# Kernel tuning notes

Hardware: AMD Instinct MI355X
Metric: run time of the kernel (lower is better)

The kernel has to match this reference:

```python
import jax, jax.numpy as jnp
import numpy as np

B, N, M, D = 2, 16384, 4096, 128  # batch, points, voxels, d_model (= d_points)


def _mlp(x, W1, b1, W2, b2):
    # Linear -> ReLU -> Linear (matches nn.Sequential(Linear, ReLU, Linear))
    return jax.nn.relu(x @ W1 + b1) @ W2 + b2


def setup_inputs() -> dict:
    key = jax.random.key(0)
    ks = jax.random.split(key, 12)
    s = 0.02
    inp = {
        "p_xyz": jax.random.normal(ks[0], (B, N, 3), jnp.float32),
        "v_xyz": jax.random.normal(ks[1], (B, 3), jnp.float32),
        "p_features": jax.random.normal(ks[2], (B, N, D), jnp.float32),
        "v_featrues": jax.random.normal(ks[3], (B, M, D), jnp.float32),
    }

    def two_layer(k, din):
        k1, k2 = jax.random.split(k)
        return (jax.random.normal(k1, (din, D), jnp.float32) * s,
                jnp.zeros((D,), jnp.float32),
                jax.random.normal(k2, (D, D), jnp.float32) * s,
                jnp.zeros((D,), jnp.float32))

    for name, din, k in (("alpha", D, ks[4]), ("beta", D, ks[5]),
                         ("omega", D, ks[6]), ("delta", 3, ks[7])):
        W1, b1, W2, b2 = two_layer(k, din)
        inp[name + "_W1"] = W1
        inp[name + "_b1"] = b1
        inp[name + "_W2"] = W2
        inp[name + "_b2"] = b2
    return inp


def reference(p_xyz, v_xyz, p_features, v_featrues,
              alpha_W1, alpha_b1, alpha_W2, alpha_b2,
              beta_W1, beta_b1, beta_W2, beta_b2,
              omega_W1, omega_b1, omega_W2, omega_b2,
              delta_W1, delta_b1, delta_W2, delta_b2):
    # dist = |p_xyz - v_xyz| per batch: [B, N, 3]
    dist = jnp.abs(p_xyz - v_xyz[:, None, :])
    pv = _mlp(dist, delta_W1, delta_b1, delta_W2, delta_b2)        # [B, N, D]
    q = _mlp(v_featrues, alpha_W1, alpha_b1, alpha_W2, alpha_b2)   # [B, M, D]
    k = _mlp(p_features, beta_W1, beta_b1, beta_W2, beta_b2)       # [B, N, D]
    v = _mlp(p_features, omega_W1, omega_b1, omega_W2, omega_b2)   # [B, N, D]
    # q@k^T + q@pv^T == q@(k+pv)^T : [B, M, N]
    scale = 1.0 / jnp.sqrt(jnp.asarray(D, dtype=q.dtype))
    scores = jnp.einsum('bmd,bnd->bmn', q, k + pv) * scale
    # softmax over dim=-2 (the query/voxel dim M), as in the original
    w = jax.nn.softmax(scores, axis=-2)                            # [B, M, N]
    res = jnp.einsum('bmn,bnd->bmd', w, v)                         # [B, M, D]
    return res + v_featrues
```

## Files before the change

### kernel.cpp

```cpp
#include <hip/hip_runtime.h>

#define B_ 2
#define N_ 16384
#define M_ 4096
#define D_ 128

typedef __attribute__((ext_vector_type(8))) short s8;
typedef __attribute__((ext_vector_type(4))) float f4;
typedef __attribute__((ext_vector_type(16))) float f16v;
typedef __attribute__((ext_vector_type(4))) unsigned short us4;
typedef unsigned short u16;

__device__ __forceinline__ u16 f2b(float f) {
  unsigned int x = __float_as_uint(f);
  unsigned int r = x + 0x7fffu + ((x >> 16) & 1u);
  return (u16)(r >> 16);
}
__device__ __forceinline__ s8 ld8(const u16* p) {
  return *reinterpret_cast<const s8*>(p);
}
__device__ __forceinline__ s8 ldcvt8(const float* p) {
  f4 x = *reinterpret_cast<const f4*>(p);
  f4 y = *reinterpret_cast<const f4*>(p + 4);
  s8 r;
  r[0] = (short)f2b(x[0]); r[1] = (short)f2b(x[1]);
  r[2] = (short)f2b(x[2]); r[3] = (short)f2b(x[3]);
  r[4] = (short)f2b(y[0]); r[5] = (short)f2b(y[1]);
  r[6] = (short)f2b(y[2]); r[7] = (short)f2b(y[3]);
  return r;
}
__device__ __forceinline__ f4 mfma16(s8 a, s8 b, f4 c) {
  return __builtin_amdgcn_mfma_f32_16x16x32_bf16(a, b, c, 0, 0, 0);
}
__device__ __forceinline__ f16v mfma32(s8 a, s8 b, f16v c) {
  return __builtin_amdgcn_mfma_f32_32x32x16_bf16(a, b, c, 0, 0, 0);
}
__device__ __forceinline__ int swz(int row, int off) {
  return (row << 8) + ((((off >> 4) ^ (row & 15)) << 4) | (off & 15));
}
#define CS 0.1275174365f

__device__ __forceinline__ void lds_barrier() {
  asm volatile("s_waitcnt lgkmcnt(0)" ::: "memory");
  __builtin_amdgcn_s_barrier();
}

__global__ __launch_bounds__(256) void wtrans(
    const float* a0, const float* a1, const float* a2, const float* a3,
    const float* a4, const float* a5, const float* a6, u16* dst) {
  const int mat = blockIdx.x >> 4, part = blockIdx.x & 15;
  const float* s;
  switch (mat) {
    case 0: s = a0; break; case 1: s = a1; break; case 2: s = a2; break;
    case 3: s = a3; break; case 4: s = a4; break; case 5: s = a5; break;
    default: s = a6; break;
  }
  u16* d = dst + mat * 16384 + part * 1024;
  const int o0 = part * 1024;
  for (int i = threadIdx.x; i < 1024; i += 256) {
    const int o = o0 + i;
    const int c = o >> 7, r = o & 127;
    d[i] = f2b(s[r * 128 + c]);
  }
}

__global__ __launch_bounds__(256) void mlps(
    const float* __restrict__ vfeat,
    const u16* __restrict__ aW1t, const float* __restrict__ ab1,
    const u16* __restrict__ aW2t, const float* __restrict__ ab2,
    u16* __restrict__ qbuf,
    const float* __restrict__ pf, const float* __restrict__ pxyz,
    const float* __restrict__ vxyz,
    const u16* __restrict__ bW1t, const float* __restrict__ bb1,
    const u16* __restrict__ bW2t, const float* __restrict__ bb2,
    const float* __restrict__ dW1, const float* __restrict__ db1,
    const u16* __restrict__ dW2t, const float* __restrict__ db2,
    const u16* __restrict__ oW1t, const float* __restrict__ ob1,
    const u16* __restrict__ oW2t, const float* __restrict__ ob2,
    u16* __restrict__ kpv_out, u16* __restrict__ vt_out) {
  __shared__ u16 H1[64][136];
  __shared__ u16 H2[64][136];
  __shared__ u16 H3[64][136];
  const int tid = threadIdx.x;
  const int wave = tid >> 6, lane = tid & 63;
  const int c16 = lane & 15, quad = lane >> 4;

  if (blockIdx.x < 256) {
    const int rowg = wave & 1, nsh = wave >> 1;
    const long row0 = (long)blockIdx.x * 32 + rowg * 16;
    s8 a[4];
    {
      const float* xr = vfeat + (row0 + c16) * D_ + quad * 8;
      #pragma unroll
      for (int kk = 0; kk < 4; kk++) a[kk] = ldcvt8(xr + kk * 32);
    }
    #pragma unroll
    for (int ns = 0; ns < 4; ns++) {
      f4 acc = {0.f, 0.f, 0.f, 0.f};
      const int c = (nsh * 4 + ns) * 16 + c16;
      const u16* wr = aW1t + (long)c * 128 + quad * 8;
      #pragma unroll
      for (int kk = 0; kk < 4; kk++) acc = mfma16(a[kk], ld8(wr + kk * 32), acc);
      const float bias = ab1[c];
      #pragma unroll
      for (int r = 0; r < 4; r++) {
        float v = acc[r] + bias;
        H1[rowg * 16 + quad * 4 + r][c] = f2b(v > 0.f ? v : 0.f);
      }
    }
    __syncthreads();
    s8 a2[4];
    #pragma unroll
    for (int kk = 0; kk < 4; kk++)
      a2[kk] = *reinterpret_cast<const s8*>(&H1[rowg * 16 + c16][kk * 32 + quad * 8]);
    #pragma unroll
    for (int ns = 0; ns < 4; ns++) {
      f4 acc = {0.f, 0.f, 0.f, 0.f};
      const int c = (nsh * 4 + ns) * 16 + c16;
      const u16* wr = aW2t + (long)c * 128 + quad * 8;
      #pragma unroll
      for (int kk = 0; kk < 4; kk++) acc = mfma16(a2[kk], ld8(wr + kk * 32), acc);
      const float bias = ab2[c];
      #pragma unroll
      for (int r = 0; r < 4; r++)
        qbuf[(row0 + quad * 4 + r) * D_ + c] = f2b(acc[r] + bias);
    }
    return;
  }
  const int bx = blockIdx.x - 256;
  const long row0 = (long)bx * 64 + wave * 16;
  s8 a[4];
  {
    const float* xr = pf + (row0 + c16) * D_ + quad * 8;
    #pragma unroll
    for (int kk = 0; kk < 4; kk++) a[kk] = ldcvt8(xr + kk * 32);
  }
  #pragma unroll
  for (int ns = 0; ns < 8; ns++) {
    f4 accb = {0.f, 0.f, 0.f, 0.f}, acco = {0.f, 0.f, 0.f, 0.f};
    const int c = ns * 16 + c16;
    const u16* wrb = bW1t + (long)c * 128 + quad * 8;
    const u16* wro = oW1t + (long)c * 128 + quad * 8;
    #pragma unroll
    for (int kk = 0; kk < 4; kk++) {
      accb = mfma16(a[kk], ld8(wrb + kk * 32), accb);
      acco = mfma16(a[kk], ld8(wro + kk * 32), acco);
    }
    const float biasb = bb1[c], biaso = ob1[c];
    #pragma unroll
    for (int r = 0; r < 4; r++) {
      float vb = accb[r] + biasb;
      float vo = acco[r] + biaso;
      H1[wave * 16 + quad * 4 + r][c] = f2b(vb > 0.f ? vb : 0.f);
      H3[wave * 16 + quad * 4 + r][c] = f2b(vo > 0.f ? vo : 0.f);
    }
  }
  {
    const long bat = ((long)bx * 64) / N_;
    const float vx0 = vxyz[bat * 3 + 0];
    const float vx1 = vxyz[bat * 3 + 1];
    const float vx2 = vxyz[bat * 3 + 2];
    for (int i = 0; i < 32; i++) {
      const int e = lane + 64 * i;
      const int rr = e >> 7, cc = e & 127;
      const long gr = row0 + rr;
      const float d0 = fabsf(pxyz[gr * 3 + 0] - vx0);
      const float d1 = fabsf(pxyz[gr * 3 + 1] - vx1);
      const float d2 = fabsf(pxyz[gr * 3 + 2] - vx2);
      float h = d0 * dW1[cc] + d1 * dW1[128 + cc] + d2 * dW1[256 + cc] + db1[cc];
      H2[wave * 16 + rr][cc] = f2b(h > 0.f ? h : 0.f);
    }
  }
  __syncthreads();
  s8 ab[4], ad[4], ao[4];
  #pragma unroll
  for (int kk = 0; kk < 4; kk++) {
    ab[kk] = *reinterpret_cast<const s8*>(&H1[wave * 16 + c16][kk * 32 + quad * 8]);
    ad[kk] = *reinterpret_cast<const s8*>(&H2[wave * 16 + c16][kk * 32 + quad * 8]);
    ao[kk] = *reinterpret_cast<const s8*>(&H3[wave * 16 + c16][kk * 32 + quad * 8]);
  }
  #pragma unroll
  for (int ns = 0; ns < 8; ns++) {
    const int c = ns * 16 + c16;
    f4 acck = {0.f, 0.f, 0.f, 0.f};
    f4 accv = {0.f, 0.f, 0.f, 0.f};
    const u16* wrb = bW2t + (long)c * 128 + quad * 8;
    const u16* wrd = dW2t + (long)c * 128 + quad * 8;
    const u16* wro = oW2t + (long)c * 128 + quad * 8;
    #pragma unroll
    for (int kk = 0; kk < 4; kk++) {
      acck = mfma16(ab[kk], ld8(wrb + kk * 32), acck);
      acck = mfma16(ad[kk], ld8(wrd + kk * 32), acck);
      accv = mfma16(ao[kk], ld8(wro + kk * 32), accv);
    }
    const float biask = bb2[c] + db2[c];
    const float biasv = ob2[c];
    #pragma unroll
    for (int r = 0; r < 4; r++)
      kpv_out[(row0 + quad * 4 + r) * D_ + c] = f2b(acck[r] + biask);
    {
      const long g = row0 + quad * 4;
      const long bb = g >> 14;
      const long n = g & (N_ - 1);
      us4 pk;
      #pragma unroll
      for (int r = 0; r < 4; r++) pk[r] = f2b(accv[r] + biasv);
      *reinterpret_cast<us4*>(vt_out + bb * (long)128 * N_ + (long)c * N_ + n) = pk;
    }
  }
}

__global__ __launch_bounds__(512, 6) void colsum_v2c(const u16* __restrict__ q,
    const u16* __restrict__ kpv, float* __restrict__ sums) {
  __shared__ char LQ[16384];
  const int tid = threadIdx.x;
  const int wave = tid >> 6, lane = tid & 63;
  const int c16 = lane & 15, quad = lane >> 4;
  const int mh = blockIdx.x & 3;
  const int nb = ((blockIdx.x >> 2) & 127) * 128 + wave * 16;
  const int b = blockIdx.x >> 9;
  const int rsub = lane >> 4, ch = lane & 15;

  s8 ak[4];
  {
    const u16* kr = kpv + ((long)b * N_ + nb + c16) * D_ + quad * 8;
    #pragma unroll
    for (int kk = 0; kk < 4; kk++) ak[kk] = ld8(kr + kk * 32);
  }
  f4 sum = {0.f, 0.f, 0.f, 0.f};
  const u16* qb = q + (long)b * M_ * D_ + (long)mh * (M_ / 4) * D_;

  for (int m0 = 0; m0 < M_ / 4; m0 += 64) {
    s8 t0 = ld8(qb + (long)(m0 + wave * 8 + rsub) * D_ + ch * 8);
    s8 t1 = ld8(qb + (long)(m0 + wave * 8 + 4 + rsub) * D_ + ch * 8);
    *reinterpret_cast<s8*>(LQ + swz(wave * 8 + rsub, ch * 16)) = t0;
    *reinterpret_cast<s8*>(LQ + swz(wave * 8 + 4 + rsub, ch * 16)) = t1;
    __syncthreads();
    #pragma unroll
    for (int ms = 0; ms < 4; ms++) {
      f4 st = {0.f, 0.f, 0.f, 0.f};
      #pragma unroll
      for (int kk = 0; kk < 4; kk++) {
        s8 bq = *reinterpret_cast<const s8*>(LQ + swz(ms * 16 + c16, kk * 64 + quad * 16));
        st = mfma16(ak[kk], bq, st);
      }
      #pragma unroll
      for (int r = 0; r < 4; r++) sum[r] += exp2f(st[r] * CS);
    }
    __syncthreads();
  }
  #pragma unroll
  for (int mask = 1; mask < 16; mask <<= 1) {
    #pragma unroll
    for (int r = 0; r < 4; r++) sum[r] += __shfl_xor(sum[r], mask, 64);
  }
  if (c16 == 0)
    *reinterpret_cast<f4*>(sums + (long)mh * (B_ * N_) + (long)b * N_ + nb + quad * 4) = sum;
}

__global__ __launch_bounds__(256) void recip_k(const float* __restrict__ sums,
                                               float* __restrict__ l2ic) {
  const int i = blockIdx.x * 256 + threadIdx.x;
  const float s = sums[i] + sums[B_ * N_ + i] + sums[2 * B_ * N_ + i]
                + sums[3 * B_ * N_ + i];
  l2ic[i] = -log2f(s);
}

__global__ __launch_bounds__(256, 4) void attn_v10(const u16* __restrict__ q,
    const u16* __restrict__ kpv, const u16* __restrict__ vt,
    const float* __restrict__ l2ic, float* __restrict__ part,
    int lgns, int nslice) {
  __shared__ char LK[16384];
  __shared__ char LP[8192];
  const int tid = threadIdx.x;
  const int wave = tid >> 6, lane = tid & 63;
  const int l31 = lane & 31, hi = lane >> 5;
  const int bid = blockIdx.x;
  const int ns = bid & ((1 << lgns) - 1);
  const int mb = (bid >> lgns) & 63;
  const int b = bid >> (lgns + 6);
  const int nt = wave & 1, mt = wave >> 1;
  const int m_base = mb * 64;
  const int n_begin = ns * nslice;
  const int rsub = lane >> 4, ch = lane & 15;

  const u16* kpb = kpv + (long)b * N_ * D_;
  const u16* vtb = vt + (long)b * (long)D_ * N_;
  const float* l2b = l2ic + (long)b * N_;

  s8 bq[8];
  {
    const u16* qr = q + ((long)b * M_ + m_base + mt * 32 + l31) * D_ + hi * 8;
    #pragma unroll
    for (int kk = 0; kk < 8; kk++) bq[kk] = ld8(qr + kk * 16);
  }
  f16v acc[2];
  #pragma unroll
  for (int i = 0; i < 2; i++)
    #pragma unroll
    for (int r = 0; r < 16; r++) acc[i][r] = 0.f;

  s8 tmp[4];
  #pragma unroll
  for (int i = 0; i < 4; i++)
    tmp[i] = ld8(kpb + (long)(n_begin + wave * 16 + i * 4 + rsub) * D_ + ch * 8);

  for (int n0 = n_begin; n0 < n_begin + nslice; n0 += 64) {
    #pragma unroll
    for (int i = 0; i < 4; i++)
      *reinterpret_cast<s8*>(LK + swz(wave * 16 + i * 4 + rsub, ch * 16)) = tmp[i];
    {
      int nn = n0 + 64;
      if (nn >= n_begin + nslice) nn = n_begin;
      #pragma unroll
      for (int i = 0; i < 4; i++)
        tmp[i] = ld8(kpb + (long)(nn + wave * 16 + i * 4 + rsub) * D_ + ch * 8);
    }
    lds_barrier();
    {
      f16v st;
      #pragma unroll
      for (int r = 0; r < 16; r++) st[r] = 0.f;
      #pragma unroll
      for (int kk = 0; kk < 8; kk++) {
        s8 aK = *reinterpret_cast<const s8*>(
            LK + swz(nt * 32 + l31, kk * 32 + hi * 16));
        st = mfma32(aK, bq[kk], st);
      }
      #pragma unroll
      for (int g = 0; g < 4; g++) {
        const f4 l2 = *reinterpret_cast<const f4*>(l2b + n0 + nt * 32 + 8 * g + 4 * hi);
        us4 pk;
        #pragma unroll
        for (int r = 0; r < 4; r++)
          pk[r] = (u16)(__float_as_uint(exp2f(fmaf(st[g * 4 + r], CS, l2[r]))) >> 16);
        *reinterpret_cast<us4*>(LP + (4 * nt + g) * 1024 + (mt * 32 + l31) * 16 + 8 * hi) = pk;
      }
    }
    lds_barrier();
    #pragma unroll
    for (int kk = 0; kk < 4; kk++) {
      s8 bv = ld8(vtb + (long)(wave * 32 + l31) * N_ + n0 + kk * 16 + hi * 8);
      #pragma unroll
      for (int i = 0; i < 2; i++) {
        s8 ap = *reinterpret_cast<const s8*>(
            LP + (2 * kk + hi) * 1024 + (i * 32 + l31) * 16);
        acc[i] = mfma32(ap, bv, acc[i]);
      }
    }
  }
  float* pt = part + (long)bid * 64 * 128;
  #pragma unroll
  for (int i = 0; i < 2; i++)
    #pragma unroll
    for (int g = 0; g < 4; g++)
      #pragma unroll
      for (int r = 0; r < 4; r++)
        pt[(i * 32 + g * 8 + 4 * hi + r) * 128 + wave * 32 + l31] = acc[i][g * 4 + r];
}

__global__ __launch_bounds__(256) void attn_reduce(const float* __restrict__ part,
    const float* __restrict__ vfeat, float* __restrict__ out, int nsplit) {
  const int g4 = blockIdx.x * 256 + threadIdx.x;
  const int b = g4 >> 17;
  const int rem = g4 & 131071;
  const int m = rem >> 5;
  const int d4 = rem & 31;
  const int mb = m >> 6, mr = m & 63;
  const long base = ((long)(b * 64 + mb) * nsplit) * 8192 + mr * 128 + d4 * 4;
  f4 s = *reinterpret_cast<const f4*>(vfeat + (long)g4 * 4);
  for (int ns = 0; ns < nsplit; ns++)
    s += *reinterpret_cast<const f4*>(part + base + ns * 8192);
  *reinterpret_cast<f4*>(out + (long)g4 * 4) = s;
}

extern "C" void kernel_launch(void* const* d_in, const int* in_sizes, int n_in,
                              void* d_out, int out_size, void* d_ws, size_t ws_size,
                              hipStream_t stream) {
  const float* p_xyz  = (const float*)d_in[0];
  const float* v_xyz  = (const float*)d_in[1];
  const float* p_feat = (const float*)d_in[2];
  const float* v_feat = (const float*)d_in[3];
  const float* aW1 = (const float*)d_in[4],  *ab1 = (const float*)d_in[5];
  const float* aW2 = (const float*)d_in[6],  *ab2 = (const float*)d_in[7];
  const float* bW1 = (const float*)d_in[8],  *bb1 = (const float*)d_in[9];
  const float* bW2 = (const float*)d_in[10], *bb2 = (const float*)d_in[11];
  const float* oW1 = (const float*)d_in[12], *ob1 = (const float*)d_in[13];
  const float* oW2 = (const float*)d_in[14], *ob2 = (const float*)d_in[15];
  const float* dW1 = (const float*)d_in[16], *db1 = (const float*)d_in[17];
  const float* dW2 = (const float*)d_in[18], *db2 = (const float*)d_in[19];

  char* ws = (char*)d_ws;
  u16* wt    = (u16*)ws;
  u16* aW1t  = wt + 0 * 16384;
  u16* aW2t  = wt + 1 * 16384;
  u16* bW1t  = wt + 2 * 16384;
  u16* bW2t  = wt + 3 * 16384;
  u16* oW1t  = wt + 4 * 16384;
  u16* oW2t  = wt + 5 * 16384;
  u16* dW2t  = wt + 6 * 16384;
  u16* qbuf  = (u16*)(ws + 262144);
  u16* kpvb  = (u16*)(ws + 2359296);
  u16* vtb   = (u16*)(ws + 10747904);
  float* invb = (float*)(ws + 19136512);
  float* partb = (float*)(ws + 19267584);
  float* sums  = partb;

  const size_t part_off = 19267584;
  int lgns = (ws_size >= part_off + (size_t)8 * B_ * M_ * D_ * 4) ? 3 : 2;
  const int nsplit = 1 << lgns;
  const int nslice = N_ / nsplit;

  wtrans<<<dim3(112), dim3(256), 0, stream>>>(aW1, aW2, bW1, bW2, oW1, oW2, dW2, wt);
  mlps<<<dim3(256 + (B_ * N_) / 64), dim3(256), 0, stream>>>(
      v_feat, aW1t, ab1, aW2t, ab2, qbuf,
      p_feat, p_xyz, v_xyz, bW1t, bb1, bW2t, bb2, dW1, db1, dW2t, db2,
      oW1t, ob1, oW2t, ob2, kpvb, vtb);
  colsum_v2c<<<dim3(B_ * 128 * 4), dim3(512), 0, stream>>>(qbuf, kpvb, sums);
  recip_k<<<dim3((B_ * N_) / 256), dim3(256), 0, stream>>>(sums, invb);
  attn_v10<<<dim3(B_ * 64 * nsplit), dim3(256), 0, stream>>>(qbuf, kpvb, vtb, invb, partb,
                                                             lgns, nslice);
  attn_reduce<<<dim3((B_ * M_ * D_ / 4) / 256), dim3(256), 0, stream>>>(partb, v_feat,
                                                                        (float*)d_out,
                                                                        nsplit);
}
```

Baseline: 329.3 us.

## Double-buffer K tiles via direct global-to-LDS loads in attention kernel

Replaces the register-staged K tile copy with __builtin_amdgcn_global_load_lds into a double-buffered LDS array, prefetching two tiles ahead and synchronising with explicit vmcnt waits and barriers. It also hoists the l2ic loads before the QK MFMAs and batches the V loads before the PV MFMAs. The aim is to cut VGPR pressure and LDS write instructions and to overlap global latency with compute. LDS use per block doubles and the hand-counted vmcnt(4) wait is fragile: if it does not match the loads actually outstanding, reads can race.

```diff
diff --git a/kernel.cpp b/kernel.cpp
--- a/kernel.cpp
+++ b/kernel.cpp
@@ -266,11 +266,26 @@
   l2ic[i] = -log2f(s);
 }
 
-__global__ __launch_bounds__(256, 4) void attn_v10(const u16* __restrict__ q,
+#define STAGE_K(bufp, nn)                                                      \
+  {                                                                            \
+    _Pragma("unroll")                                                          \
+    for (int i_ = 0; i_ < 4; i_++) {                                           \
+      const int row_ = wave * 16 + i_ * 4 + rsub;                              \
+      const u16* src_ = kpb + (long)((nn) + row_) * D_ + ((ch ^ (row_ & 15)) * 8); \
+      char* dst_ = (bufp) + wave * 4096 + i_ * 1024;                           \
+      __builtin_amdgcn_global_load_lds(                                        \
+          (const __attribute__((address_space(1))) void*)src_,                 \
+          (__attribute__((address_space(3))) void*)dst_, 16, 0, 0);            \
+    }                                                                          \
+  }
+
+__global__ __launch_bounds__(256)
+__attribute__((amdgpu_waves_per_eu(4, 4)))
+void attn_v11(const u16* __restrict__ q,
     const u16* __restrict__ kpv, const u16* __restrict__ vt,
     const float* __restrict__ l2ic, float* __restrict__ part,
     int lgns, int nslice) {
-  __shared__ char LK[16384];
+  __shared__ char LK[2][16384];
   __shared__ char LP[8192];
   const int tid = threadIdx.x;
   const int wave = tid >> 6, lane = tid & 63;
@@ -282,6 +297,7 @@
   const int nt = wave & 1, mt = wave >> 1;
   const int m_base = mb * 64;
   const int n_begin = ns * nslice;
+  const int n_end = n_begin + nslice;
   const int rsub = lane >> 4, ch = lane & 15;
 
   const u16* kpb = kpv + (long)b * N_ * D_;
@@ -300,53 +316,57 @@
     #pragma unroll
     for (int r = 0; r < 16; r++) acc[i][r] = 0.f;
 
-  s8 tmp[4];
-  #pragma unroll
-  for (int i = 0; i < 4; i++)
-    tmp[i] = ld8(kpb + (long)(n_begin + wave * 16 + i * 4 + rsub) * D_ + ch * 8);
-
-  for (int n0 = n_begin; n0 < n_begin + nslice; n0 += 64) {
-    #pragma unroll
-    for (int i = 0; i < 4; i++)
-      *reinterpret_cast<s8*>(LK + swz(wave * 16 + i * 4 + rsub, ch * 16)) = tmp[i];
+  STAGE_K(LK[0], n_begin);
+  STAGE_K(LK[1], n_begin + 64);
+
+  int it = 0;
+  for (int n0 = n_begin; n0 < n_end; n0 += 64, ++it) {
+    char* lkc = LK[it & 1];
+    asm volatile("s_waitcnt vmcnt(4) lgkmcnt(0)" ::: "memory");
+    __builtin_amdgcn_s_barrier();
     {
-      int nn = n0 + 64;
-      if (nn >= n_begin + nslice) nn = n_begin;
-      #pragma unroll
-      for (int i = 0; i < 4; i++)
-        tmp[i] = ld8(kpb + (long)(nn + wave * 16 + i * 4 + rsub) * D_ + ch * 8);
-    }
-    lds_barrier();
-    {
+      f4 l2v[4];
+      #pragma unroll
+      for (int g = 0; g < 4; g++)
+        l2v[g] = *reinterpret_cast<const f4*>(l2b + n0 + nt * 32 + 8 * g + 4 * hi);
       f16v st;
       #pragma unroll
       for (int r = 0; r < 16; r++) st[r] = 0.f;
       #pragma unroll
       for (int kk = 0; kk < 8; kk++) {
         s8 aK = *reinterpret_cast<const s8*>(
-            LK + swz(nt * 32 + l31, kk * 32 + hi * 16));
+            lkc + swz(nt * 32 + l31, kk * 32 + hi * 16));
         st = mfma32(aK, bq[kk], st);
       }
       #pragma unroll
       for (int g = 0; g < 4; g++) {
-        const f4 l2 = *reinterpret_cast<const f4*>(l2b + n0 + nt * 32 + 8 * g + 4 * hi);
         us4 pk;
         #pragma unroll
         for (int r = 0; r < 4; r++)
-          pk[r] = (u16)(__float_as_uint(exp2f(fmaf(st[g * 4 + r], CS, l2[r]))) >> 16);
+          pk[r] = (u16)(__float_as_uint(exp2f(fmaf(st[g * 4 + r], CS, l2v[g][r]))) >> 16);
         *reinterpret_cast<us4*>(LP + (4 * nt + g) * 1024 + (mt * 32 + l31) * 16 + 8 * hi) = pk;
       }
     }
     lds_barrier();
-    #pragma unroll
-    for (int kk = 0; kk < 4; kk++) {
-      s8 bv = ld8(vtb + (long)(wave * 32 + l31) * N_ + n0 + kk * 16 + hi * 8);
-      #pragma unroll
-      for (int i = 0; i < 2; i++) {
-        s8 ap = *reinterpret_cast<const s8*>(
-            LP + (2 * kk + hi) * 1024 + (i * 32 + l31) * 16);
-        acc[i] = mfma32(ap, bv, acc[i]);
+    {
+      s8 bv[4];
+      #pragma unroll
+      for (int kk = 0; kk < 4; kk++)
+        bv[kk] = ld8(vtb + (long)(wave * 32 + l31) * N_ + n0 + kk * 16 + hi * 8);
+      #pragma unroll
+      for (int kk = 0; kk < 4; kk++) {
+        #pragma unroll
+        for (int i = 0; i < 2; i++) {
+          s8 ap = *reinterpret_cast<const s8*>(
+              LP + (2 * kk + hi) * 1024 + (i * 32 + l31) * 16);
+          acc[i] = mfma32(ap, bv[kk], acc[i]);
+        }
       }
+    }
+    {
+      int nn = n0 + 128;
+      if (nn >= n_end) nn = n_begin;
+      STAGE_K(lkc, nn);
     }
   }
   float* pt = part + (long)bid * 64 * 128;
@@ -418,7 +438,7 @@
       oW1t, ob1, oW2t, ob2, kpvb, vtb);
   colsum_v2c<<<dim3(B_ * 128 * 4), dim3(512), 0, stream>>>(qbuf, kpvb, sums);
   recip_k<<<dim3((B_ * N_) / 256), dim3(256), 0, stream>>>(sums, invb);
-  attn_v10<<<dim3(B_ * 64 * nsplit), dim3(256), 0, stream>>>(qbuf, kpvb, vtb, invb, partb,
+  attn_v11<<<dim3(B_ * 64 * nsplit), dim3(256), 0, stream>>>(qbuf, kpvb, vtb, invb, partb,
                                                              lgns, nslice);
   attn_reduce<<<dim3((B_ * M_ * D_ / 4) / 256), dim3(256), 0, stream>>>(partb, v_feat,
                                                                         (float*)d_out,
```

Measured after the change: 332.8 us. About the same (+1.1%).

## Shrink attention M-tile to 32 and switch to 16x16 MFMA with higher occupancy

Applied to the files above, without the earlier changes.

The attention kernel now processes 32 voxel rows per block instead of 64 and uses 16x16x32 MFMA tiles instead of 32x32. The P staging buffer is halved and gets an XOR swizzle, and a waves_per_eu hint targets 6-8 waves per SIMD. The grid doubles, which means more blocks and higher occupancy to hide the latency of K and V loads. The cost is that each block now reloads the K/V tiles for half as many queries, doubling global K/V traffic per query. The reduce kernel's indexing is updated to the new partial layout.

```diff
diff --git a/kernel.cpp b/kernel.cpp
--- a/kernel.cpp
+++ b/kernel.cpp
@@ -266,21 +266,24 @@
   l2ic[i] = -log2f(s);
 }
 
-__global__ __launch_bounds__(256, 4) void attn_v10(const u16* __restrict__ q,
+__global__ __launch_bounds__(256)
+__attribute__((amdgpu_waves_per_eu(6, 8)))
+void attn_v12(const u16* __restrict__ q,
     const u16* __restrict__ kpv, const u16* __restrict__ vt,
     const float* __restrict__ l2ic, float* __restrict__ part,
     int lgns, int nslice) {
   __shared__ char LK[16384];
-  __shared__ char LP[8192];
+  __shared__ char LP[4096];
   const int tid = threadIdx.x;
   const int wave = tid >> 6, lane = tid & 63;
-  const int l31 = lane & 31, hi = lane >> 5;
+  const int c16 = lane & 15, quad = lane >> 4;
   const int bid = blockIdx.x;
   const int ns = bid & ((1 << lgns) - 1);
-  const int mb = (bid >> lgns) & 63;
-  const int b = bid >> (lgns + 6);
-  const int nt = wave & 1, mt = wave >> 1;
-  const int m_base = mb * 64;
+  const int mb = (bid >> lgns) & 127;
+  const int b = bid >> (lgns + 7);
+  const int u = wave & 1;
+  const int tpair = wave >> 1;
+  const int m_base = mb * 32;
   const int n_begin = ns * nslice;
   const int rsub = lane >> 4, ch = lane & 15;
 
@@ -288,17 +291,17 @@
   const u16* vtb = vt + (long)b * (long)D_ * N_;
   const float* l2b = l2ic + (long)b * N_;
 
-  s8 bq[8];
+  s8 bq[4];
   {
-    const u16* qr = q + ((long)b * M_ + m_base + mt * 32 + l31) * D_ + hi * 8;
-    #pragma unroll
-    for (int kk = 0; kk < 8; kk++) bq[kk] = ld8(qr + kk * 16);
-  }
-  f16v acc[2];
+    const u16* qr = q + ((long)b * M_ + m_base + u * 16 + c16) * D_ + quad * 8;
+    #pragma unroll
+    for (int kk = 0; kk < 4; kk++) bq[kk] = ld8(qr + kk * 32);
+  }
+  f4 acc[2][2];
   #pragma unroll
   for (int i = 0; i < 2; i++)
     #pragma unroll
-    for (int r = 0; r < 16; r++) acc[i][r] = 0.f;
+    for (int v = 0; v < 2; v++) acc[i][v] = f4{0.f, 0.f, 0.f, 0.f};
 
   s8 tmp[4];
   #pragma unroll
@@ -317,46 +320,56 @@
         tmp[i] = ld8(kpb + (long)(nn + wave * 16 + i * 4 + rsub) * D_ + ch * 8);
     }
     lds_barrier();
+    #pragma unroll
+    for (int j = 0; j < 2; j++) {
+      const int t = tpair * 2 + j;
+      f4 st = {0.f, 0.f, 0.f, 0.f};
+      #pragma unroll
+      for (int kk = 0; kk < 4; kk++) {
+        s8 aK = *reinterpret_cast<const s8*>(
+            LK + swz(t * 16 + c16, kk * 64 + quad * 16));
+        st = mfma16(aK, bq[kk], st);
+      }
+      const f4 l2 = *reinterpret_cast<const f4*>(l2b + n0 + t * 16 + quad * 4);
+      us4 pk;
+      #pragma unroll
+      for (int r = 0; r < 4; r++)
+        pk[r] = (u16)(__float_as_uint(exp2f(fmaf(st[r], CS, l2[r]))) >> 16);
+      const int mrow = u * 16 + c16;
+      *reinterpret_cast<us4*>(
+          LP + mrow * 128 + ((t * 32 + quad * 8) ^ ((c16 & 7) << 4))) = pk;
+    }
+    lds_barrier();
     {
-      f16v st;
-      #pragma unroll
-      for (int r = 0; r < 16; r++) st[r] = 0.f;
-      #pragma unroll
-      for (int kk = 0; kk < 8; kk++) {
-        s8 aK = *reinterpret_cast<const s8*>(
-            LK + swz(nt * 32 + l31, kk * 32 + hi * 16));
-        st = mfma32(aK, bq[kk], st);
+      s8 bv[2][2];
+      #pragma unroll
+      for (int v = 0; v < 2; v++)
+        #pragma unroll
+        for (int ks = 0; ks < 2; ks++)
+          bv[v][ks] = ld8(vtb + (long)(wave * 32 + v * 16 + c16) * N_
+                          + n0 + ks * 32 + quad * 8);
+      #pragma unroll
+      for (int ks = 0; ks < 2; ks++) {
+        #pragma unroll
+        for (int i = 0; i < 2; i++) {
+          const int m = i * 16 + c16;
+          s8 ap = *reinterpret_cast<const s8*>(
+              LP + m * 128 + ((ks * 64 + quad * 16) ^ ((c16 & 7) << 4)));
+          #pragma unroll
+          for (int v = 0; v < 2; v++)
+            acc[i][v] = mfma16(ap, bv[v][ks], acc[i][v]);
+        }
       }
-      #pragma unroll
-      for (int g = 0; g < 4; g++) {
-        const f4 l2 = *reinterpret_cast<const f4*>(l2b + n0 + nt * 32 + 8 * g + 4 * hi);
-        us4 pk;
-        #pragma unroll
-        for (int r = 0; r < 4; r++)
-          pk[r] = (u16)(__float_as_uint(exp2f(fmaf(st[g * 4 + r], CS, l2[r]))) >> 16);
-        *reinterpret_cast<us4*>(LP + (4 * nt + g) * 1024 + (mt * 32 + l31) * 16 + 8 * hi) = pk;
-      }
-    }
-    lds_barrier();
-    #pragma unroll
-    for (int kk = 0; kk < 4; kk++) {
-      s8 bv = ld8(vtb + (long)(wave * 32 + l31) * N_ + n0 + kk * 16 + hi * 8);
-      #pragma unroll
-      for (int i = 0; i < 2; i++) {
-        s8 ap = *reinterpret_cast<const s8*>(
-            LP + (2 * kk + hi) * 1024 + (i * 32 + l31) * 16);
-        acc[i] = mfma32(ap, bv, acc[i]);
-      }
-    }
-  }
-  float* pt = part + (long)bid * 64 * 128;
+    }
+  }
+  float* pt = part + (long)bid * 32 * 128;
   #pragma unroll
   for (int i = 0; i < 2; i++)
     #pragma unroll
-    for (int g = 0; g < 4; g++)
+    for (int v = 0; v < 2; v++)
       #pragma unroll
       for (int r = 0; r < 4; r++)
-        pt[(i * 32 + g * 8 + 4 * hi + r) * 128 + wave * 32 + l31] = acc[i][g * 4 + r];
+        pt[(i * 16 + quad * 4 + r) * 128 + wave * 32 + v * 16 + c16] = acc[i][v][r];
 }
 
 __global__ __launch_bounds__(256) void attn_reduce(const float* __restrict__ part,
@@ -366,11 +379,11 @@
   const int rem = g4 & 131071;
   const int m = rem >> 5;
   const int d4 = rem & 31;
-  const int mb = m >> 6, mr = m & 63;
-  const long base = ((long)(b * 64 + mb) * nsplit) * 8192 + mr * 128 + d4 * 4;
+  const int mb = m >> 5, mr = m & 31;
+  const long base = ((long)(b * 128 + mb) * nsplit) * 4096 + mr * 128 + d4 * 4;
   f4 s = *reinterpret_cast<const f4*>(vfeat + (long)g4 * 4);
   for (int ns = 0; ns < nsplit; ns++)
-    s += *reinterpret_cast<const f4*>(part + base + ns * 8192);
+    s += *reinterpret_cast<const f4*>(part + base + ns * 4096);
   *reinterpret_cast<f4*>(out + (long)g4 * 4) = s;
 }
 
@@ -418,8 +431,8 @@
       oW1t, ob1, oW2t, ob2, kpvb, vtb);
   colsum_v2c<<<dim3(B_ * 128 * 4), dim3(512), 0, stream>>>(qbuf, kpvb, sums);
   recip_k<<<dim3((B_ * N_) / 256), dim3(256), 0, stream>>>(sums, invb);
-  attn_v10<<<dim3(B_ * 64 * nsplit), dim3(256), 0, stream>>>(qbuf, kpvb, vtb, invb, partb,
-                                                             lgns, nslice);
+  attn_v12<<<dim3(B_ * 128 * nsplit), dim3(256), 0, stream>>>(qbuf, kpvb, vtb, invb,
+                                                              partb, lgns, nslice);
   attn_reduce<<<dim3((B_ * M_ * D_ / 4) / 256), dim3(256), 0, stream>>>(partb, v_feat,
                                                                         (float*)d_out,
                                                                         nsplit);
```

Result: slower. 504.7 us (+53.2%).

## Double attention M-tile to 128 rows per block to reuse K/V loads

Applied to the files above, without the earlier changes.

Each attention block now covers 128 query rows instead of 64, so each wave computes two score tiles against the same K fragment and four PV accumulators against the same V fragment. The V fragment loads are hoisted ahead of the score computation so they overlap with it. This halves K/V global traffic per output row and the grid size. In exchange it raises register pressure (occupancy hint lowered from 4 to 2), doubles the P buffer in LDS, halves the number of blocks, and requires the reduce kernel's indexing to change to match.

```diff
diff --git a/kernel.cpp b/kernel.cpp
--- a/kernel.cpp
+++ b/kernel.cpp
@@ -266,21 +266,21 @@
   l2ic[i] = -log2f(s);
 }
 
-__global__ __launch_bounds__(256, 4) void attn_v10(const u16* __restrict__ q,
+__global__ __launch_bounds__(256, 2) void attn_v13(const u16* __restrict__ q,
     const u16* __restrict__ kpv, const u16* __restrict__ vt,
     const float* __restrict__ l2ic, float* __restrict__ part,
     int lgns, int nslice) {
   __shared__ char LK[16384];
-  __shared__ char LP[8192];
+  __shared__ char LP[16384];
   const int tid = threadIdx.x;
   const int wave = tid >> 6, lane = tid & 63;
   const int l31 = lane & 31, hi = lane >> 5;
   const int bid = blockIdx.x;
   const int ns = bid & ((1 << lgns) - 1);
-  const int mb = (bid >> lgns) & 63;
-  const int b = bid >> (lgns + 6);
-  const int nt = wave & 1, mt = wave >> 1;
-  const int m_base = mb * 64;
+  const int mb = (bid >> lgns) & 31;
+  const int b = bid >> (lgns + 5);
+  const int nt = wave & 1, mth = wave >> 1;
+  const int m_base = mb * 128;
   const int n_begin = ns * nslice;
   const int rsub = lane >> 4, ch = lane & 15;
 
@@ -288,15 +288,16 @@
   const u16* vtb = vt + (long)b * (long)D_ * N_;
   const float* l2b = l2ic + (long)b * N_;
 
-  s8 bq[8];
-  {
-    const u16* qr = q + ((long)b * M_ + m_base + mt * 32 + l31) * D_ + hi * 8;
-    #pragma unroll
-    for (int kk = 0; kk < 8; kk++) bq[kk] = ld8(qr + kk * 16);
-  }
-  f16v acc[2];
-  #pragma unroll
-  for (int i = 0; i < 2; i++)
+  s8 bq[2][8];
+  #pragma unroll
+  for (int t = 0; t < 2; t++) {
+    const u16* qr = q + ((long)b * M_ + m_base + (mth + 2 * t) * 32 + l31) * D_ + hi * 8;
+    #pragma unroll
+    for (int kk = 0; kk < 8; kk++) bq[t][kk] = ld8(qr + kk * 16);
+  }
+  f16v acc[4];
+  #pragma unroll
+  for (int i = 0; i < 4; i++)
     #pragma unroll
     for (int r = 0; r < 16; r++) acc[i][r] = 0.f;
 
@@ -317,41 +318,50 @@
         tmp[i] = ld8(kpb + (long)(nn + wave * 16 + i * 4 + rsub) * D_ + ch * 8);
     }
     lds_barrier();
+    s8 bv[4];
+    #pragma unroll
+    for (int kk = 0; kk < 4; kk++)
+      bv[kk] = ld8(vtb + (long)(wave * 32 + l31) * N_ + n0 + kk * 16 + hi * 8);
     {
-      f16v st;
-      #pragma unroll
-      for (int r = 0; r < 16; r++) st[r] = 0.f;
+      f16v st0, st1;
+      #pragma unroll
+      for (int r = 0; r < 16; r++) { st0[r] = 0.f; st1[r] = 0.f; }
       #pragma unroll
       for (int kk = 0; kk < 8; kk++) {
         s8 aK = *reinterpret_cast<const s8*>(
             LK + swz(nt * 32 + l31, kk * 32 + hi * 16));
-        st = mfma32(aK, bq[kk], st);
+        st0 = mfma32(aK, bq[0][kk], st0);
+        st1 = mfma32(aK, bq[1][kk], st1);
       }
       #pragma unroll
       for (int g = 0; g < 4; g++) {
         const f4 l2 = *reinterpret_cast<const f4*>(l2b + n0 + nt * 32 + 8 * g + 4 * hi);
-        us4 pk;
+        us4 pk0, pk1;
         #pragma unroll
-        for (int r = 0; r < 4; r++)
-          pk[r] = (u16)(__float_as_uint(exp2f(fmaf(st[g * 4 + r], CS, l2[r]))) >> 16);
-        *reinterpret_cast<us4*>(LP + (4 * nt + g) * 1024 + (mt * 32 + l31) * 16 + 8 * hi) = pk;
+        for (int r = 0; r < 4; r++) {
+          pk0[r] = (u16)(__float_as_uint(exp2f(fmaf(st0[g * 4 + r], CS, l2[r]))) >> 16);
+          pk1[r] = (u16)(__float_as_uint(exp2f(fmaf(st1[g * 4 + r], CS, l2[r]))) >> 16);
+        }
+        *reinterpret_cast<us4*>(LP + (4 * nt + g) * 2048
+                                + ((mth + 0) * 32 + l31) * 16 + 8 * hi) = pk0;
+        *reinterpret_cast<us4*>(LP + (4 * nt + g) * 2048
+                                + ((mth + 2) * 32 + l31) * 16 + 8 * hi) = pk1;
       }
     }
     lds_barrier();
     #pragma unroll
     for (int kk = 0; kk < 4; kk++) {
-      s8 bv = ld8(vtb + (long)(wave * 32 + l31) * N_ + n0 + kk * 16 + hi * 8);
-      #pragma unroll
-      for (int i = 0; i < 2; i++) {
+      #pragma unroll
+      for (int i = 0; i < 4; i++) {
         s8 ap = *reinterpret_cast<const s8*>(
-            LP + (2 * kk + hi) * 1024 + (i * 32 + l31) * 16);
-        acc[i] = mfma32(ap, bv, acc[i]);
+            LP + (2 * kk + hi) * 2048 + (i * 32 + l31) * 16);
+        acc[i] = mfma32(ap, bv[kk], acc[i]);
       }
     }
   }
-  float* pt = part + (long)bid * 64 * 128;
-  #pragma unroll
-  for (int i = 0; i < 2; i++)
+  float* pt = part + (long)bid * 128 * 128;
+  #pragma unroll
+  for (int i = 0; i < 4; i++)
     #pragma unroll
     for (int g = 0; g < 4; g++)
       #pragma unroll
@@ -366,11 +376,11 @@
   const int rem = g4 & 131071;
   const int m = rem >> 5;
   const int d4 = rem & 31;
-  const int mb = m >> 6, mr = m & 63;
-  const long base = ((long)(b * 64 + mb) * nsplit) * 8192 + mr * 128 + d4 * 4;
+  const int mb = m >> 7, mr = m & 127;
+  const long base = ((long)(b * 32 + mb) * nsplit) * 16384 + mr * 128 + d4 * 4;
   f4 s = *reinterpret_cast<const f4*>(vfeat + (long)g4 * 4);
   for (int ns = 0; ns < nsplit; ns++)
-    s += *reinterpret_cast<const f4*>(part + base + ns * 8192);
+    s += *reinterpret_cast<const f4*>(part + base + ns * 16384);
   *reinterpret_cast<f4*>(out + (long)g4 * 4) = s;
 }
 
@@ -418,8 +428,8 @@
       oW1t, ob1, oW2t, ob2, kpvb, vtb);
   colsum_v2c<<<dim3(B_ * 128 * 4), dim3(512), 0, stream>>>(qbuf, kpvb, sums);
   recip_k<<<dim3((B_ * N_) / 256), dim3(256), 0, stream>>>(sums, invb);
-  attn_v10<<<dim3(B_ * 64 * nsplit), dim3(256), 0, stream>>>(qbuf, kpvb, vtb, invb, partb,
-                                                             lgns, nslice);
+  attn_v13<<<dim3(B_ * 32 * nsplit), dim3(256), 0, stream>>>(qbuf, kpvb, vtb, invb,
+                                                             partb, lgns, nslice);
   attn_reduce<<<dim3((B_ * M_ * D_ / 4) / 256), dim3(256), 0, stream>>>(partb, v_feat,
                                                                         (float*)d_out,
                                                                         nsplit);
```

Result: faster. 289.5 us (-12.1%).
